# Kernel optimization log

Hardware: AMD Instinct MI355X
Metric: run time of the kernel (lower is better)

Reference implementation:

```python
import jax, jax.numpy as jnp
import numpy as np

CODEBOOK_SIZE = 512
LATENT_DIM = 12
BATCH = 512
TOKENS = 256


def setup_inputs() -> dict:
    key = jax.random.key(0)
    k1, k2 = jax.random.split(key)
    x = jax.random.normal(k1, (BATCH, TOKENS, LATENT_DIM), dtype=jnp.float32)
    # nn.Embedding init: uniform(-1/K, 1/K)
    lim = 1.0 / CODEBOOK_SIZE
    codebook = jax.random.uniform(k2, (CODEBOOK_SIZE, LATENT_DIM), dtype=jnp.float32,
                                  minval=-lim, maxval=lim)
    return {"x": x, "codebook": codebook}


def reference(x, codebook):
    # same as for torch.cdist (sqrt is monotonic).
    x2 = jnp.sum(x * x, axis=-1, keepdims=True)            # [B, N, 1]
    w2 = jnp.sum(codebook * codebook, axis=-1)             # [K]
    xw = jnp.einsum('bnd,kd->bnk', x, codebook)            # [B, N, K]
    dist2 = x2 - 2.0 * xw + w2                             # [B, N, K]
    indices = jnp.argmin(dist2, axis=-1)                   # [B, N] int
    quantized = codebook[indices]                          # [B, N, D]

    codebook_loss = jnp.mean((quantized - jax.lax.stop_gradient(x)) ** 2)
    commitment_loss = 0.25 * jnp.mean((jax.lax.stop_gradient(quantized) - x) ** 2)
    quantize_loss = codebook_loss + commitment_loss

    # straight-through estimator
    quantized_st = x + jax.lax.stop_gradient(quantized - x)
    return quantized_st, indices, quantize_loss
```

## Files before the change

kernel.cpp:

```cpp
#include <hip/hip_runtime.h>
#include <math.h>

namespace {
constexpr int KCB   = 512;
constexpr int DIM   = 12;
constexpr int NTOK  = 512 * 256;
constexpr int QSIZE = NTOK * DIM;
constexpr int NSPLIT = 8;
constexpr int KCHUNK = KCB / NSPLIT;
constexpr int TPT    = 4;
constexpr int TOKS_PER_BLOCK = 64 * TPT;
constexpr int NBLK   = NTOK / TOKS_PER_BLOCK;

__device__ inline unsigned long long mkkey(float v, int k) {
    unsigned su = __float_as_uint(v);
    su = (su & 0x80000000u) ? ~su : (su | 0x80000000u);
    return ((unsigned long long)su << 32) | (unsigned)k;
}

__device__ inline float bcast(float v, int lane) {
    return __uint_as_float(__builtin_amdgcn_readlane(__float_as_uint(v), lane));
}

__global__ void init_loss(float* __restrict__ out) {
    if (threadIdx.x == 0) out[QSIZE + NTOK] = 0.f;
}

__global__ __launch_bounds__(512, 4) void vq_main(const float* __restrict__ x,
                                                  const float* __restrict__ cb,
                                                  float* __restrict__ out) {
    __shared__ unsigned long long keys[NSPLIT * TOKS_PER_BLOCK];
    __shared__ float lred[TPT];
    const int tid  = threadIdx.x;
    const int lane = tid & 63;
    const int s = __builtin_amdgcn_readfirstlane(tid >> 6);
    const int tbase = blockIdx.x * TOKS_PER_BLOCK;

    float cw[13];
    {
        const int kc = (s << 6) + lane;
        const float4* wp = (const float4*)(cb + (size_t)kc * DIM);
        float4 c0 = wp[0], c1 = wp[1], c2 = wp[2];
        cw[0] = c0.x; cw[1] = c0.y; cw[2]  = c0.z; cw[3]  = c0.w;
        cw[4] = c1.x; cw[5] = c1.y; cw[6]  = c1.z; cw[7]  = c1.w;
        cw[8] = c2.x; cw[9] = c2.y; cw[10] = c2.z; cw[11] = c2.w;
        float w2 = 0.f;
#pragma unroll
        for (int d = 0; d < DIM; ++d) w2 = fmaf(cw[d], cw[d], w2);
        cw[12] = w2;
    }

    float xs[TPT][DIM];
    float x2[TPT];
#pragma unroll
    for (int j = 0; j < TPT; ++j) {
        const float4* xp = (const float4*)(x + (size_t)(tbase + j * 64 + lane) * DIM);
        float4 a0 = xp[0], a1 = xp[1], a2 = xp[2];
        xs[j][0] = a0.x; xs[j][1] = a0.y; xs[j][2]  = a0.z; xs[j][3]  = a0.w;
        xs[j][4] = a1.x; xs[j][5] = a1.y; xs[j][6]  = a1.z; xs[j][7]  = a1.w;
        xs[j][8] = a2.x; xs[j][9] = a2.y; xs[j][10] = a2.z; xs[j][11] = a2.w;
        float t2 = 0.f;
#pragma unroll
        for (int d = 0; d < DIM; ++d) t2 = fmaf(xs[j][d], xs[j][d], t2);
        x2[j] = t2;
    }

    float best[TPT];
    int   bi[TPT];
#pragma unroll
    for (int j = 0; j < TPT; ++j) { best[j] = INFINITY; bi[j] = 0; }

    const int k0 = s << 6;

#pragma unroll 8
    for (int kk = 0; kk < KCHUNK; ++kk) {
        float w[13];
#pragma unroll
        for (int d = 0; d < 13; ++d) w[d] = bcast(cw[d], kk);
        const int k = k0 + kk;
#pragma unroll
        for (int j = 0; j < TPT; ++j) {
            float xw = 0.f;
            xw = fmaf(xs[j][0],  w[0],  xw);
            xw = fmaf(xs[j][1],  w[1],  xw);
            xw = fmaf(xs[j][2],  w[2],  xw);
            xw = fmaf(xs[j][3],  w[3],  xw);
            xw = fmaf(xs[j][4],  w[4],  xw);
            xw = fmaf(xs[j][5],  w[5],  xw);
            xw = fmaf(xs[j][6],  w[6],  xw);
            xw = fmaf(xs[j][7],  w[7],  xw);
            xw = fmaf(xs[j][8],  w[8],  xw);
            xw = fmaf(xs[j][9],  w[9],  xw);
            xw = fmaf(xs[j][10], w[10], xw);
            xw = fmaf(xs[j][11], w[11], xw);
            float d = fmaf(-2.f, xw, x2[j]) + w[12];
            bool c = d < best[j];
            best[j] = c ? d : best[j];
            bi[j]   = c ? k : bi[j];
        }
    }

#pragma unroll
    for (int j = 0; j < TPT; ++j)
        keys[s * TOKS_PER_BLOCK + j * 64 + lane] = mkkey(best[j], bi[j]);
    __syncthreads();

    if (s < TPT) {
        const int tok = s * 64 + lane;
        unsigned long long m = keys[tok];
#pragma unroll
        for (int r = 1; r < NSPLIT; ++r) {
            unsigned long long v = keys[r * TOKS_PER_BLOCK + tok];
            m = v < m ? v : m;
        }
        const int bid = (int)(m & 0xffffffffULL);
        unsigned eu = (unsigned)(m >> 32);
        unsigned orig = (eu & 0x80000000u) ? (eu ^ 0x80000000u) : ~eu;
        const float bsc = __uint_as_float(orig);
        const int t = tbase + tok;

        float xv[DIM];
#pragma unroll
        for (int j = 0; j < TPT; ++j)
            if (j == s) {
#pragma unroll
                for (int d = 0; d < DIM; ++d) xv[d] = xs[j][d];
            }

        const float4* wrow = (const float4*)(cb + (size_t)bid * DIM);
        float4 q0 = wrow[0], q1 = wrow[1], q2 = wrow[2];
        float qs[DIM] = {q0.x, q0.y, q0.z, q0.w, q1.x, q1.y, q1.z, q1.w,
                         q2.x, q2.y, q2.z, q2.w};

        float4* qo = (float4*)(out + (size_t)t * DIM);
        float4 r0, r1, r2;
        r0.x = xv[0] + (qs[0] - xv[0]);    r0.y = xv[1] + (qs[1] - xv[1]);
        r0.z = xv[2] + (qs[2] - xv[2]);    r0.w = xv[3] + (qs[3] - xv[3]);
        r1.x = xv[4] + (qs[4] - xv[4]);    r1.y = xv[5] + (qs[5] - xv[5]);
        r1.z = xv[6] + (qs[6] - xv[6]);    r1.w = xv[7] + (qs[7] - xv[7]);
        r2.x = xv[8] + (qs[8] - xv[8]);    r2.y = xv[9] + (qs[9] - xv[9]);
        r2.z = xv[10] + (qs[10] - xv[10]); r2.w = xv[11] + (qs[11] - xv[11]);
        qo[0] = r0; qo[1] = r1; qo[2] = r2;

        out[QSIZE + t] = (float)bid;

        float ls = bsc * (1.25f / (float)QSIZE);
#pragma unroll
        for (int off = 32; off > 0; off >>= 1) ls += __shfl_down(ls, off);
        if (lane == 0) lred[s] = ls;
    }
    __syncthreads();
    if (tid == 0) atomicAdd(out + QSIZE + NTOK, lred[0] + lred[1] + lred[2] + lred[3]);
}
}

extern "C" void kernel_launch(void* const* d_in, const int* in_sizes, int n_in,
                              void* d_out, int out_size, void* d_ws, size_t ws_size,
                              hipStream_t stream) {
    const float* x  = (const float*)d_in[0];
    const float* cb = (const float*)d_in[1];
    float* out = (float*)d_out;
    (void)d_ws; (void)ws_size;

    init_loss<<<1, 64, 0, stream>>>(out);
    vq_main<<<NBLK, 512, 0, stream>>>(x, cb, out);
}
```

Baseline: 95.97 us.

## Stream packed codebook rows via double-buffered scalar loads, one token per lane

A pre-pass kernel packs each codebook row into 16 floats with its squared norm. The main kernel then gives each lane a single token and splits the codebook across 4 waves. Each wave streams rows through double-buffered inline-asm s_load_dwordx16 into scalar registers, replacing the readlane broadcasts of per-lane codebook registers. The loss is now written as per-block partials and summed by a separate deterministic reduce kernel instead of atomics. The cost is two extra launches and less register-level token reuse per codebook fetch, since each wave now handles one token per lane instead of four.

Result: slower. 104.3 us (+8.7%).

```diff
diff --git a/kernel.cpp b/kernel.cpp
--- a/kernel.cpp
+++ b/kernel.cpp
@@ -6,11 +6,14 @@
 constexpr int DIM   = 12;
 constexpr int NTOK  = 512 * 256;
 constexpr int QSIZE = NTOK * DIM;
-constexpr int NSPLIT = 8;
-constexpr int KCHUNK = KCB / NSPLIT;
-constexpr int TPT    = 4;
-constexpr int TOKS_PER_BLOCK = 64 * TPT;
-constexpr int NBLK   = NTOK / TOKS_PER_BLOCK;
+constexpr int KSPLIT = 4;
+constexpr int KCHUNK = KCB / KSPLIT;
+constexpr int TPB    = 256;
+constexpr int NBLK   = NTOK / 64;
+constexpr int ROWF   = 16;
+constexpr int PARTIALS_OFF = 16384;
+
+typedef __attribute__((ext_vector_type(16))) float f32x16;
 
 __device__ inline unsigned long long mkkey(float v, int k) {
     unsigned su = __float_as_uint(v);
@@ -18,139 +21,151 @@
     return ((unsigned long long)su << 32) | (unsigned)k;
 }
 
-__device__ inline float bcast(float v, int lane) {
-    return __uint_as_float(__builtin_amdgcn_readlane(__float_as_uint(v), lane));
+__global__ __launch_bounds__(256) void pack_cb(const float* __restrict__ cb,
+                                               float* __restrict__ pk) {
+    int k = blockIdx.x * blockDim.x + threadIdx.x;
+    if (k >= KCB) return;
+    float w[DIM];
+#pragma unroll
+    for (int d = 0; d < DIM; ++d) w[d] = cb[k * DIM + d];
+    float w2 = 0.f;
+#pragma unroll
+    for (int d = 0; d < DIM; ++d) w2 = fmaf(w[d], w[d], w2);
+#pragma unroll
+    for (int d = 0; d < DIM; ++d) pk[k * ROWF + d] = w[d];
+    pk[k * ROWF + 12] = w2;
+    pk[k * ROWF + 13] = 0.f; pk[k * ROWF + 14] = 0.f; pk[k * ROWF + 15] = 0.f;
 }
 
-__global__ void init_loss(float* __restrict__ out) {
-    if (threadIdx.x == 0) out[QSIZE + NTOK] = 0.f;
-}
+#define SCORE_CODE(R, KIDX)                                                  \
+    {                                                                        \
+        const int kq_ = (KIDX);                                              \
+        float xw = 0.f;                                                      \
+        xw = fmaf(xs[0],  (R)[0],  xw);                                      \
+        xw = fmaf(xs[1],  (R)[1],  xw);                                      \
+        xw = fmaf(xs[2],  (R)[2],  xw);                                      \
+        xw = fmaf(xs[3],  (R)[3],  xw);                                      \
+        xw = fmaf(xs[4],  (R)[4],  xw);                                      \
+        xw = fmaf(xs[5],  (R)[5],  xw);                                      \
+        xw = fmaf(xs[6],  (R)[6],  xw);                                      \
+        xw = fmaf(xs[7],  (R)[7],  xw);                                      \
+        xw = fmaf(xs[8],  (R)[8],  xw);                                      \
+        xw = fmaf(xs[9],  (R)[9],  xw);                                      \
+        xw = fmaf(xs[10], (R)[10], xw);                                      \
+        xw = fmaf(xs[11], (R)[11], xw);                                      \
+        float dq = fmaf(-2.f, xw, x2) + (R)[12];                             \
+        bool cq = dq < best;               \
+        best = cq ? dq : best;                                               \
+        bi   = cq ? kq_ : bi;                                                \
+    }
 
-__global__ __launch_bounds__(512, 4) void vq_main(const float* __restrict__ x,
+#define SISSUE(R, ADDR)                                                      \
+    asm volatile("s_load_dwordx16 %0, %1, 0" : "=s"(R) : "s"(ADDR));
+#define SWAIT(R)                                                             \
+    asm volatile("s_waitcnt lgkmcnt(0)" : "+s"(R));
+
+__global__ __launch_bounds__(256, 4) void vq_main(const float* __restrict__ x,
                                                   const float* __restrict__ cb,
-                                                  float* __restrict__ out) {
-    __shared__ unsigned long long keys[NSPLIT * TOKS_PER_BLOCK];
-    __shared__ float lred[TPT];
+                                                  const float* __restrict__ pk,
+                                                  float* __restrict__ out,
+                                                  float* __restrict__ partials) {
+    __shared__ unsigned long long keys[KSPLIT * 64];
     const int tid  = threadIdx.x;
     const int lane = tid & 63;
-    const int s = __builtin_amdgcn_readfirstlane(tid >> 6);
-    const int tbase = blockIdx.x * TOKS_PER_BLOCK;
+    const int w = __builtin_amdgcn_readfirstlane(tid >> 6);
+    const int tok = blockIdx.x * 64 + lane;
 
-    float cw[13];
+    float xs[DIM];
+    float x2;
     {
-        const int kc = (s << 6) + lane;
-        const float4* wp = (const float4*)(cb + (size_t)kc * DIM);
-        float4 c0 = wp[0], c1 = wp[1], c2 = wp[2];
-        cw[0] = c0.x; cw[1] = c0.y; cw[2]  = c0.z; cw[3]  = c0.w;
-        cw[4] = c1.x; cw[5] = c1.y; cw[6]  = c1.z; cw[7]  = c1.w;
-        cw[8] = c2.x; cw[9] = c2.y; cw[10] = c2.z; cw[11] = c2.w;
-        float w2 = 0.f;
+        const float4* xp = (const float4*)(x + (size_t)tok * DIM);
+        float4 a0 = xp[0], a1 = xp[1], a2 = xp[2];
+        xs[0] = a0.x; xs[1] = a0.y; xs[2]  = a0.z; xs[3]  = a0.w;
+        xs[4] = a1.x; xs[5] = a1.y; xs[6]  = a1.z; xs[7]  = a1.w;
+        xs[8] = a2.x; xs[9] = a2.y; xs[10] = a2.z; xs[11] = a2.w;
+        float t2 = 0.f;
 #pragma unroll
-        for (int d = 0; d < DIM; ++d) w2 = fmaf(cw[d], cw[d], w2);
-        cw[12] = w2;
+        for (int d = 0; d < DIM; ++d) t2 = fmaf(xs[d], xs[d], t2);
+        x2 = t2;
     }
 
-    float xs[TPT][DIM];
-    float x2[TPT];
-#pragma unroll
-    for (int j = 0; j < TPT; ++j) {
-        const float4* xp = (const float4*)(x + (size_t)(tbase + j * 64 + lane) * DIM);
-        float4 a0 = xp[0], a1 = xp[1], a2 = xp[2];
-        xs[j][0] = a0.x; xs[j][1] = a0.y; xs[j][2]  = a0.z; xs[j][3]  = a0.w;
-        xs[j][4] = a1.x; xs[j][5] = a1.y; xs[j][6]  = a1.z; xs[j][7]  = a1.w;
-        xs[j][8] = a2.x; xs[j][9] = a2.y; xs[j][10] = a2.z; xs[j][11] = a2.w;
-        float t2 = 0.f;
-#pragma unroll
-        for (int d = 0; d < DIM; ++d) t2 = fmaf(xs[j][d], xs[j][d], t2);
-        x2[j] = t2;
+    float best = INFINITY;
+    int   bi = 0;
+
+    const int k0 = w * KCHUNK;
+    const unsigned long long base =
+        (unsigned long long)(uintptr_t)(pk + (size_t)k0 * ROWF);
+
+    f32x16 A, B;
+    SISSUE(A, base);
+    for (int kk = 0; kk < KCHUNK - 2; kk += 2) {
+        SWAIT(A);
+        SISSUE(B, base + (unsigned long long)((kk + 1) * 64));
+        SCORE_CODE(A, k0 + kk);
+        SWAIT(B);
+        SISSUE(A, base + (unsigned long long)((kk + 2) * 64));
+        SCORE_CODE(B, k0 + kk + 1);
     }
+    SWAIT(A);
+    SISSUE(B, base + (unsigned long long)((KCHUNK - 1) * 64));
+    SCORE_CODE(A, k0 + KCHUNK - 2);
+    SWAIT(B);
+    SCORE_CODE(B, k0 + KCHUNK - 1);
 
-    float best[TPT];
-    int   bi[TPT];
-#pragma unroll
-    for (int j = 0; j < TPT; ++j) { best[j] = INFINITY; bi[j] = 0; }
-
-    const int k0 = s << 6;
-
-#pragma unroll 8
-    for (int kk = 0; kk < KCHUNK; ++kk) {
-        float w[13];
-#pragma unroll
-        for (int d = 0; d < 13; ++d) w[d] = bcast(cw[d], kk);
-        const int k = k0 + kk;
-#pragma unroll
-        for (int j = 0; j < TPT; ++j) {
-            float xw = 0.f;
-            xw = fmaf(xs[j][0],  w[0],  xw);
-            xw = fmaf(xs[j][1],  w[1],  xw);
-            xw = fmaf(xs[j][2],  w[2],  xw);
-            xw = fmaf(xs[j][3],  w[3],  xw);
-            xw = fmaf(xs[j][4],  w[4],  xw);
-            xw = fmaf(xs[j][5],  w[5],  xw);
-            xw = fmaf(xs[j][6],  w[6],  xw);
-            xw = fmaf(xs[j][7],  w[7],  xw);
-            xw = fmaf(xs[j][8],  w[8],  xw);
-            xw = fmaf(xs[j][9],  w[9],  xw);
-            xw = fmaf(xs[j][10], w[10], xw);
-            xw = fmaf(xs[j][11], w[11], xw);
-            float d = fmaf(-2.f, xw, x2[j]) + w[12];
-            bool c = d < best[j];
-            best[j] = c ? d : best[j];
-            bi[j]   = c ? k : bi[j];
-        }
-    }
-
-#pragma unroll
-    for (int j = 0; j < TPT; ++j)
-        keys[s * TOKS_PER_BLOCK + j * 64 + lane] = mkkey(best[j], bi[j]);
+    keys[w * 64 + lane] = mkkey(best, bi);
     __syncthreads();
 
-    if (s < TPT) {
-        const int tok = s * 64 + lane;
-        unsigned long long m = keys[tok];
+    if (tid < 64) {
+        unsigned long long m = keys[lane];
 #pragma unroll
-        for (int r = 1; r < NSPLIT; ++r) {
-            unsigned long long v = keys[r * TOKS_PER_BLOCK + tok];
+        for (int r = 1; r < KSPLIT; ++r) {
+            unsigned long long v = keys[r * 64 + lane];
             m = v < m ? v : m;
         }
         const int bid = (int)(m & 0xffffffffULL);
         unsigned eu = (unsigned)(m >> 32);
         unsigned orig = (eu & 0x80000000u) ? (eu ^ 0x80000000u) : ~eu;
         const float bsc = __uint_as_float(orig);
-        const int t = tbase + tok;
-
-        float xv[DIM];
-#pragma unroll
-        for (int j = 0; j < TPT; ++j)
-            if (j == s) {
-#pragma unroll
-                for (int d = 0; d < DIM; ++d) xv[d] = xs[j][d];
-            }
 
         const float4* wrow = (const float4*)(cb + (size_t)bid * DIM);
         float4 q0 = wrow[0], q1 = wrow[1], q2 = wrow[2];
         float qs[DIM] = {q0.x, q0.y, q0.z, q0.w, q1.x, q1.y, q1.z, q1.w,
                          q2.x, q2.y, q2.z, q2.w};
 
-        float4* qo = (float4*)(out + (size_t)t * DIM);
+        float4* qo = (float4*)(out + (size_t)tok * DIM);
         float4 r0, r1, r2;
-        r0.x = xv[0] + (qs[0] - xv[0]);    r0.y = xv[1] + (qs[1] - xv[1]);
-        r0.z = xv[2] + (qs[2] - xv[2]);    r0.w = xv[3] + (qs[3] - xv[3]);
-        r1.x = xv[4] + (qs[4] - xv[4]);    r1.y = xv[5] + (qs[5] - xv[5]);
-        r1.z = xv[6] + (qs[6] - xv[6]);    r1.w = xv[7] + (qs[7] - xv[7]);
-        r2.x = xv[8] + (qs[8] - xv[8]);    r2.y = xv[9] + (qs[9] - xv[9]);
-        r2.z = xv[10] + (qs[10] - xv[10]); r2.w = xv[11] + (qs[11] - xv[11]);
+        r0.x = xs[0] + (qs[0] - xs[0]);    r0.y = xs[1] + (qs[1] - xs[1]);
+        r0.z = xs[2] + (qs[2] - xs[2]);    r0.w = xs[3] + (qs[3] - xs[3]);
+        r1.x = xs[4] + (qs[4] - xs[4]);    r1.y = xs[5] + (qs[5] - xs[5]);
+        r1.z = xs[6] + (qs[6] - xs[6]);    r1.w = xs[7] + (qs[7] - xs[7]);
+        r2.x = xs[8] + (qs[8] - xs[8]);    r2.y = xs[9] + (qs[9] - xs[9]);
+        r2.z = xs[10] + (qs[10] - xs[10]); r2.w = xs[11] + (qs[11] - xs[11]);
         qo[0] = r0; qo[1] = r1; qo[2] = r2;
 
-        out[QSIZE + t] = (float)bid;
+        out[QSIZE + tok] = (float)bid;
 
         float ls = bsc * (1.25f / (float)QSIZE);
 #pragma unroll
         for (int off = 32; off > 0; off >>= 1) ls += __shfl_down(ls, off);
-        if (lane == 0) lred[s] = ls;
+        if (lane == 0) partials[blockIdx.x] = ls;
     }
+}
+
+__global__ __launch_bounds__(512) void reduce_loss(const float* __restrict__ partials,
+                                                   float* __restrict__ out) {
+    __shared__ float r[8];
+    float v = (partials[threadIdx.x]        + partials[threadIdx.x + 512])
+            + (partials[threadIdx.x + 1024] + partials[threadIdx.x + 1536]);
+#pragma unroll
+    for (int off = 32; off > 0; off >>= 1) v += __shfl_down(v, off);
+    if ((threadIdx.x & 63) == 0) r[threadIdx.x >> 6] = v;
     __syncthreads();
-    if (tid == 0) atomicAdd(out + QSIZE + NTOK, lred[0] + lred[1] + lred[2] + lred[3]);
+    if (threadIdx.x == 0) {
+        float t = 0.f;
+#pragma unroll
+        for (int i = 0; i < 8; ++i) t += r[i];
+        out[QSIZE + NTOK] = t;
+    }
 }
 }
 
@@ -160,8 +175,10 @@
     const float* x  = (const float*)d_in[0];
     const float* cb = (const float*)d_in[1];
     float* out = (float*)d_out;
-    (void)d_ws; (void)ws_size;
+    float* pk  = (float*)d_ws;
+    float* partials = (float*)d_ws + PARTIALS_OFF;
 
-    init_loss<<<1, 64, 0, stream>>>(out);
-    vq_main<<<NBLK, 512, 0, stream>>>(x, cb, out);
+    pack_cb<<<2, 256, 0, stream>>>(cb, pk);
+    vq_main<<<NBLK, TPB, 0, stream>>>(x, cb, pk, out, partials);
+    reduce_loss<<<1, 512, 0, stream>>>(partials, out);
 }
```
